# Performance work log

Hardware: AMD Instinct MI355X
Metric: run time of the kernel (lower is better)

## Reference

```python
import jax, jax.numpy as jnp
import numpy as np

B, CD, NF, V, D = 16384, 13, 26, 100000, 64
BOT = [256, 128]
TOP = [512, 256, 128]
NUM_EMB = NF + 1            # 27 (bottom output + 26 categorical)
NUM_INTER = NUM_EMB * (NUM_EMB - 1) // 2  # 351
TOP_IN = NUM_INTER + NUM_EMB * D          # 2079
BN_INV = 1.0 / np.sqrt(1.0 + 1e-5)        # eval-mode BatchNorm: running_mean=0, running_var=1


def _lin(key, fan_in, fan_out):
    kw, kb = jax.random.split(key)
    s = 1.0 / np.sqrt(fan_in)
    W = jax.random.uniform(kw, (fan_in, fan_out), minval=-s, maxval=s, dtype=jnp.float32)
    b = jax.random.uniform(kb, (fan_out,), minval=-s, maxval=s, dtype=jnp.float32)
    return W, b


def setup_inputs() -> dict:
    key = jax.random.key(0)
    ks = jax.random.split(key, 16)
    continuous = jax.random.normal(ks[0], (B, CD), dtype=jnp.float32)
    cat_idx = jax.random.randint(ks[1], (B, NF), 0, V, dtype=jnp.int32)
    emb_tables = jax.random.normal(ks[2], (NF, V, D), dtype=jnp.float32)  # nn.Embedding init ~ N(0,1)
    W1, b1 = _lin(ks[3], CD, BOT[0]);   g1 = jnp.ones((BOT[0],)); be1 = jnp.zeros((BOT[0],))
    W2, b2 = _lin(ks[4], BOT[0], BOT[1]); g2 = jnp.ones((BOT[1],)); be2 = jnp.zeros((BOT[1],))
    W3, b3 = _lin(ks[5], BOT[1], D)
    W4, b4 = _lin(ks[6], TOP_IN, TOP[0]); g4 = jnp.ones((TOP[0],)); be4 = jnp.zeros((TOP[0],))
    W5, b5 = _lin(ks[7], TOP[0], TOP[1]); g5 = jnp.ones((TOP[1],)); be5 = jnp.zeros((TOP[1],))
    W6, b6 = _lin(ks[8], TOP[1], TOP[2]); g6 = jnp.ones((TOP[2],)); be6 = jnp.zeros((TOP[2],))
    W7, b7 = _lin(ks[9], TOP[2], 1)
    return dict(continuous=continuous, cat_idx=cat_idx, emb_tables=emb_tables,
                W1=W1, b1=b1, g1=g1, be1=be1, W2=W2, b2=b2, g2=g2, be2=be2, W3=W3, b3=b3,
                W4=W4, b4=b4, g4=g4, be4=be4, W5=W5, b5=b5, g5=g5, be5=be5,
                W6=W6, b6=b6, g6=g6, be6=be6, W7=W7, b7=b7)


def _bn(x, g, b):
    # eval-mode BatchNorm1d with running_mean=0, running_var=1
    return g * (x * BN_INV) + b


def reference(continuous, cat_idx, emb_tables,
              W1, b1, g1, be1, W2, b2, g2, be2, W3, b3,
              W4, b4, g4, be4, W5, b5, g5, be5, W6, b6, g6, be6, W7, b7):
    # Bottom MLP: 13 -> 256 -> 128 -> 64
    h = jax.nn.relu(_bn(continuous @ W1 + b1, g1, be1))
    h = jax.nn.relu(_bn(h @ W2 + b2, g2, be2))
    bottom = h @ W3 + b3                         # [B, D]

    # Embedding gather: one table per categorical feature
    emb = emb_tables[jnp.arange(NF), cat_idx]    # [B, NF, D]
    all_emb = jnp.concatenate([bottom[:, None, :], emb], axis=1)  # [B, 27, D]

    # Pairwise dot-product interactions via one bmm + triu gather
    Z = jnp.einsum('bnd,bmd->bnm', all_emb, all_emb)              # [B, 27, 27]
    iu, ju = np.triu_indices(NUM_EMB, k=1)                        # row-major i<j (matches torch loop order)
    inter = Z[:, iu, ju]                                          # [B, 351]

    top_in = jnp.concatenate([inter, all_emb.reshape(all_emb.shape[0], -1)], axis=1)  # [B, 2079]

    # Top MLP: 2079 -> 512 -> 256 -> 128 -> 1
    t = jax.nn.relu(_bn(top_in @ W4 + b4, g4, be4))
    t = jax.nn.relu(_bn(t @ W5 + b5, g5, be5))
    t = jax.nn.relu(_bn(t @ W6 + b6, g6, be6))
    scores = t @ W7 + b7                                          # [B, 1]
    return scores
```

## Files before the change

kernel.cpp:

```cpp
#include <hip/hip_runtime.h>
#include <stdint.h>
#include <stddef.h>

#define BATCH   16384
#define CDIM    13
#define NFEAT   26
#define VROWS   100000
#define EDIM    64
#define NEMB    27
#define NINTER  351
#define TOPIN   2079
#define KP4     2112
#define BN_INVF 0.9999950000374997f

typedef __attribute__((ext_vector_type(8)))  __bf16 bf16x8;
typedef __attribute__((ext_vector_type(4)))  float  f32x4;
typedef __attribute__((ext_vector_type(16))) float  f32x16;
typedef __attribute__((ext_vector_type(4)))  uint32_t uint4v;

__device__ __forceinline__ uint32_t f2bf(float f){
  uint32_t u = __float_as_uint(f);
  return (u + 0x7fffu + ((u >> 16) & 1u)) >> 16;
}
__device__ __forceinline__ float bf2f(uint32_t h){ return __uint_as_float(h << 16); }
__device__ __forceinline__ uint32_t pack2(float a, float b){
  return f2bf(a) | (f2bf(b) << 16);
}
__device__ __forceinline__ void async_load16(const void* g, void* l){
  __builtin_amdgcn_global_load_lds(
      (const __attribute__((address_space(1))) uint32_t*)g,
      (__attribute__((address_space(3))) uint32_t*)l, 16, 0, 0);
}
__device__ __forceinline__ int rswz(int row){ return ((row ^ (row >> 3)) & 7) << 3; }

__device__ __forceinline__ void transpose_tile(
    float (*tile)[65], const float* __restrict__ src, unsigned short* __restrict__ dst,
    int K, int N, int Kpad, int remap, int kb, int nb){
  int k0 = kb*64, n0 = nb*64, t = threadIdx.x;
  int srcBase = remap ? ((k0 < 1728) ? (k0 + 351) : (k0 - 1728)) : k0;
  #pragma unroll 4
  for(int p = 0; p < 16; p++){
    int kr = p*4 + (t >> 6), nc = t & 63;
    float v = 0.f;
    if(k0 + kr < K && (n0 + nc) < N) v = src[(size_t)(srcBase + kr) * N + n0 + nc];
    tile[kr][nc] = v;
  }
  __syncthreads();
  #pragma unroll 4
  for(int p = 0; p < 16; p++){
    int nr = p*4 + (t >> 6), kc = t & 63;
    if(k0 + kc < Kpad && (n0 + nr) < N)
      dst[(size_t)(n0 + nr) * Kpad + k0 + kc] = (unsigned short)f2bf(tile[kc][nr]);
  }
}

__global__ __launch_bounds__(256) void prep(
    const float* __restrict__ W1, const float* __restrict__ W2, const float* __restrict__ W3,
    const float* __restrict__ W4, const float* __restrict__ W5, const float* __restrict__ W6,
    unsigned short* __restrict__ W1t, unsigned short* __restrict__ W2t,
    unsigned short* __restrict__ W3t, unsigned short* __restrict__ W4t,
    unsigned short* __restrict__ W5t, unsigned short* __restrict__ W6t){
  __shared__ float tile[64][65];
  int bid = blockIdx.x;
  if(bid < 264){ transpose_tile(tile, W4, W4t, TOPIN, 512, KP4, 1, bid % 33, bid / 33); }
  else if(bid < 296){ int r = bid-264; transpose_tile(tile, W5, W5t, 512, 256, 512, 0, r % 8, r / 8); }
  else if(bid < 304){ int r = bid-296; transpose_tile(tile, W6, W6t, 256, 128, 256, 0, r % 4, r / 4); }
  else if(bid < 312){ int r = bid-304; transpose_tile(tile, W2, W2t, 256, 128, 256, 0, r % 4, r / 4); }
  else if(bid < 314){ int r = bid-312; transpose_tile(tile, W3, W3t, 128, 64, 128, 0, r, 0); }
  else               { int r = bid-314; transpose_tile(tile, W1, W1t, CDIM, 256, 32, 0, 0, r); }
}

__global__ __launch_bounds__(256) void bottom_interact(
    const float* __restrict__ cont, const int* __restrict__ cat_idx,
    const float* __restrict__ emb,
    const unsigned short* __restrict__ W1t, const unsigned short* __restrict__ W2t,
    const unsigned short* __restrict__ W3t,
    const float* __restrict__ b1, const float* __restrict__ g1, const float* __restrict__ be1,
    const float* __restrict__ b2, const float* __restrict__ g2, const float* __restrict__ be2,
    const float* __restrict__ b3,
    unsigned short* __restrict__ top_in){
  __shared__ unsigned short h1hi[16*256];
  __shared__ unsigned short h1lo[16*256];
  __shared__ unsigned short h2hi[16*128];
  __shared__ unsigned short h2lo[16*128];
  __shared__ unsigned short bot_s[16*64];
  __shared__ unsigned short inter_s[16][352];
  int t = threadIdx.x, w = t >> 6, l = t & 63;
  int m0 = blockIdx.x * 16;
  int lr = l & 15, lg = l >> 4, lk = lg * 8;
  int r = l & 31, h = l >> 5;
  bool activeB = (r >= 1 && r < NEMB);

  int idx4[4];
  #pragma unroll
  for(int s = 0; s < 4; s++){
    int b = m0 + w*4 + s;
    idx4[s] = activeB ? cat_idx[b*NFEAT + (r-1)] : 0;
  }

  bf16x8 axh, axl;
  {
    uint32_t uh[4], ul[4];
    #pragma unroll
    for(int p = 0; p < 4; p++){
      float x0 = 0.f, x1 = 0.f;
      int k0 = lk + 2*p;
      if(k0 < CDIM)     x0 = cont[(size_t)(m0 + lr)*CDIM + k0];
      if(k0 + 1 < CDIM) x1 = cont[(size_t)(m0 + lr)*CDIM + k0 + 1];
      uint32_t h0 = f2bf(x0), h1b = f2bf(x1);
      uh[p] = h0 | (h1b << 16);
      ul[p] = f2bf(x0 - bf2f(h0)) | (f2bf(x1 - bf2f(h1b)) << 16);
    }
    uint4v vh, vl;
    #pragma unroll
    for(int e = 0; e < 4; e++){ vh[e] = uh[e]; vl[e] = ul[e]; }
    axh = __builtin_bit_cast(bf16x8, vh);
    axl = __builtin_bit_cast(bf16x8, vl);
  }

  {
    #pragma unroll
    for(int nt = 0; nt < 4; nt++){
      int n = w*64 + nt*16 + lr;
      bf16x8 bw = *(const bf16x8*)(W1t + (size_t)n*32 + lk);
      f32x4 acc;
      #pragma unroll
      for(int e = 0; e < 4; e++) acc[e] = 0.f;
      acc = __builtin_amdgcn_mfma_f32_16x16x32_bf16(axh, bw, acc, 0, 0, 0);
      acc = __builtin_amdgcn_mfma_f32_16x16x32_bf16(axl, bw, acc, 0, 0, 0);
      float sc = g1[n]*BN_INVF, bo = be1[n], bi = b1[n];
      #pragma unroll
      for(int q = 0; q < 4; q++){
        int ro = lg*4 + q;
        float y = fmaxf(sc*(acc[q] + bi) + bo, 0.f);
        uint32_t hb = f2bf(y);
        int idx = ro*256 + (n ^ rswz(ro));
        h1hi[idx] = (unsigned short)hb;
        h1lo[idx] = (unsigned short)f2bf(y - bf2f(hb));
      }
    }
  }
  __syncthreads();

  {
    f32x4 acc[2];
    #pragma unroll
    for(int nt = 0; nt < 2; nt++)
      #pragma unroll
      for(int e = 0; e < 4; e++) acc[nt][e] = 0.f;
    for(int ks = 0; ks < 8; ks++){
      bf16x8 bw[2];
      #pragma unroll
      for(int nt = 0; nt < 2; nt++){
        int n = w*32 + nt*16 + lr;
        bw[nt] = *(const bf16x8*)(W2t + (size_t)n*256 + ks*32 + lk);
      }
      int ai = lr*256 + ((ks*32 + lk) ^ rswz(lr));
      bf16x8 ah = *(const bf16x8*)(h1hi + ai);
      bf16x8 al = *(const bf16x8*)(h1lo + ai);
      #pragma unroll
      for(int nt = 0; nt < 2; nt++){
        acc[nt] = __builtin_amdgcn_mfma_f32_16x16x32_bf16(ah, bw[nt], acc[nt], 0, 0, 0);
        acc[nt] = __builtin_amdgcn_mfma_f32_16x16x32_bf16(al, bw[nt], acc[nt], 0, 0, 0);
      }
    }
    #pragma unroll
    for(int nt = 0; nt < 2; nt++){
      int n = w*32 + nt*16 + lr;
      float sc = g2[n]*BN_INVF, bo = be2[n], bi = b2[n];
      #pragma unroll
      for(int q = 0; q < 4; q++){
        int ro = lg*4 + q;
        float y = fmaxf(sc*(acc[nt][q] + bi) + bo, 0.f);
        uint32_t hb = f2bf(y);
        int idx = ro*128 + (n ^ rswz(ro));
        h2hi[idx] = (unsigned short)hb;
        h2lo[idx] = (unsigned short)f2bf(y - bf2f(hb));
      }
    }
  }
  __syncthreads();

  {
    f32x4 acc;
    #pragma unroll
    for(int e = 0; e < 4; e++) acc[e] = 0.f;
    int n = w*16 + lr;
    for(int ks = 0; ks < 4; ks++){
      bf16x8 bw = *(const bf16x8*)(W3t + (size_t)n*128 + ks*32 + lk);
      int ai = lr*128 + ((ks*32 + lk) ^ rswz(lr));
      bf16x8 ah = *(const bf16x8*)(h2hi + ai);
      bf16x8 al = *(const bf16x8*)(h2lo + ai);
      acc = __builtin_amdgcn_mfma_f32_16x16x32_bf16(ah, bw, acc, 0, 0, 0);
      acc = __builtin_amdgcn_mfma_f32_16x16x32_bf16(al, bw, acc, 0, 0, 0);
    }
    float bi = b3[n];
    #pragma unroll
    for(int q = 0; q < 4; q++){
      int ro = lg*4 + q;
      bot_s[ro*64 + n] = (unsigned short)f2bf(acc[q] + bi);
    }
  }
  __syncthreads();

  for(int s = 0; s < 4; s++){
    int sb = w*4 + s;
    int b = m0 + sb;
    uint4v q[4];
    if(r == 0){
      #pragma unroll
      for(int p = 0; p < 4; p++)
        q[p] = *(const uint4v*)(bot_s + sb*64 + h*8 + p*16);
    } else if(activeB){
      const float* src = emb + ((size_t)(r-1)*VROWS + (size_t)idx4[s])*64;
      #pragma unroll
      for(int p = 0; p < 4; p++){
        int k0 = h*8 + p*16;
        float4 v0 = *(const float4*)(src + k0);
        float4 v1 = *(const float4*)(src + k0 + 4);
        q[p][0] = pack2(v0.x, v0.y); q[p][1] = pack2(v0.z, v0.w);
        q[p][2] = pack2(v1.x, v1.y); q[p][3] = pack2(v1.z, v1.w);
      }
    } else {
      #pragma unroll
      for(int p = 0; p < 4; p++){ q[p][0]=0; q[p][1]=0; q[p][2]=0; q[p][3]=0; }
    }
    if(r < NEMB){
      #pragma unroll
      for(int p = 0; p < 4; p++)
        *(uint4v*)(top_in + (size_t)b*KP4 + r*64 + h*8 + p*16) = q[p];
    }
    f32x16 acc;
    #pragma unroll
    for(int i = 0; i < 16; i++) acc[i] = 0.f;
    #pragma unroll
    for(int p = 0; p < 4; p++){
      bf16x8 a = __builtin_bit_cast(bf16x8, q[p]);
      acc = __builtin_amdgcn_mfma_f32_32x32x16_bf16(a, a, acc, 0, 0, 0);
    }
    if(r < NEMB){
      #pragma unroll
      for(int qq = 0; qq < 16; qq++){
        int i = (qq & 3) + 8*(qq >> 2) + 4*h;
        if(i < r){
          int p = i*(53 - i)/2 + (r - i - 1);
          inter_s[sb][p] = (unsigned short)f2bf(acc[qq]);
        }
      }
    }
    asm volatile("s_waitcnt lgkmcnt(0)" ::: "memory");
    size_t basei = (size_t)b*KP4 + 1728;
    for(int t0 = l; t0 < 176; t0 += 64){
      uint32_t lo = inter_s[sb][2*t0];
      uint32_t hi = (2*t0 + 1 < NINTER) ? (uint32_t)inter_s[sb][2*t0 + 1] : 0u;
      *(uint32_t*)(top_in + basei + 2*t0) = lo | (hi << 16);
    }
    if(l < 16) *(uint32_t*)(top_in + (size_t)b*KP4 + 2080 + 2*l) = 0;
  }
}

template<int KSTEPS, int NB>
__global__ __launch_bounds__(512, 2) void gemm_deep(
    const unsigned short* __restrict__ A, int sA,
    const unsigned short* __restrict__ Bw, int sB,
    const float* __restrict__ bias, const float* __restrict__ gg,
    const float* __restrict__ be,
    unsigned short* __restrict__ out, int sOut){
  __shared__ char smem[3*49152];
  int nwg = gridDim.x;
  int bid = blockIdx.x;
  int lin = (bid & 7) * (nwg >> 3) + (bid >> 3);
  int m0 = (lin / NB) * 256, n0 = (lin % NB) * 128;
  int t = threadIdx.x, w = t >> 6, l = t & 63;
  int wr = (w >> 1) * 64, wc = (w & 1) * 64;
  int l31 = l & 31, l5 = l >> 5;
  f32x16 acc[2][2];
  #pragma unroll
  for(int i = 0; i < 2; i++)
    #pragma unroll
    for(int j = 0; j < 2; j++)
      #pragma unroll
      for(int e = 0; e < 16; e++) acc[i][j][e] = 0.f;

  const unsigned short* g[6];
  int ldsOff[6];
  #pragma unroll
  for(int i = 0; i < 6; i++){
    if(i < 4){
      int o = i*8192 + t*16;
      int row = o >> 7;
      int cb  = (o & 127) ^ ((row & 7) << 4);
      g[i] = A + (size_t)(m0 + row)*sA + (cb >> 1);
      ldsOff[i] = o;
    } else {
      int o = (i-4)*8192 + t*16;
      int row = o >> 7;
      int cb  = (o & 127) ^ ((row & 7) << 4);
      g[i] = Bw + (size_t)(n0 + row)*sB + (cb >> 1);
      ldsOff[i] = 32768 + o;
    }
  }
  int swz = (l31 & 7) << 4;

  #pragma unroll
  for(int i = 0; i < 6; i++) async_load16(g[i], smem + ldsOff[i]);
  #pragma unroll
  for(int i = 0; i < 6; i++) async_load16(g[i] + 64, smem + 49152 + ldsOff[i]);
  asm volatile("s_waitcnt vmcnt(6)" ::: "memory");
  __builtin_amdgcn_s_barrier();

  for(int kt = 0; kt < KSTEPS; kt++){
    int cur = kt % 3;
    int nxt2 = (kt + 2) % 3;
    int ksrc = (kt + 2 < KSTEPS) ? (kt + 2) : (KSTEPS - 1);
    const char* bA = smem + cur*49152;
    const char* bB = bA + 32768;
    #pragma unroll
    for(int ph = 0; ph < 2; ph++){
      if(ph == 0){
        #pragma unroll
        for(int i = 0; i < 3; i++)
          async_load16(g[i] + ksrc*64, smem + nxt2*49152 + ldsOff[i]);
      } else {
        #pragma unroll
        for(int i = 3; i < 6; i++)
          async_load16(g[i] + ksrc*64, smem + nxt2*49152 + ldsOff[i]);
      }
      bf16x8 af[2][2], bfr[2][2];
      #pragma unroll
      for(int ks = 0; ks < 2; ks++){
        int ko = ((ph*2 + ks)*32 + l5*16) ^ swz;
        #pragma unroll
        for(int mt = 0; mt < 2; mt++)
          af[ks][mt]  = *(const bf16x8*)(bA + (wr + mt*32 + l31)*128 + ko);
        #pragma unroll
        for(int nt = 0; nt < 2; nt++)
          bfr[ks][nt] = *(const bf16x8*)(bB + (wc + nt*32 + l31)*128 + ko);
      }
      if(ph == 1) asm volatile("s_waitcnt vmcnt(6)" ::: "memory");
      __builtin_amdgcn_s_barrier();
      __builtin_amdgcn_s_setprio(1);
      #pragma unroll
      for(int ks = 0; ks < 2; ks++)
        #pragma unroll
        for(int mt = 0; mt < 2; mt++)
          #pragma unroll
          for(int nt = 0; nt < 2; nt++)
            acc[mt][nt] = __builtin_amdgcn_mfma_f32_32x32x16_bf16(af[ks][mt], bfr[ks][nt], acc[mt][nt], 0, 0, 0);
      __builtin_amdgcn_s_setprio(0);
      __builtin_amdgcn_s_barrier();
    }
  }

  #pragma unroll
  for(int mt = 0; mt < 2; mt++){
    #pragma unroll
    for(int nt = 0; nt < 2; nt++){
      int col = n0 + wc + nt*32 + l31;
      float sc = gg[col]*BN_INVF, bo = be[col], bi = bias[col];
      #pragma unroll
      for(int reg = 0; reg < 16; reg++){
        int rowf = (reg & 3) + 8*(reg >> 2) + 4*l5;
        int row = m0 + wr + mt*32 + rowf;
        float y = fmaxf(sc*(acc[mt][nt][reg] + bi) + bo, 0.f);
        out[(size_t)row*sOut + col] = (unsigned short)f2bf(y);
      }
    }
  }
}

__global__ __launch_bounds__(256) void gemm_tail(
    const unsigned short* __restrict__ h4,
    const unsigned short* __restrict__ W5t,
    const float* __restrict__ b5, const float* __restrict__ g5, const float* __restrict__ be5,
    const unsigned short* __restrict__ W6t,
    const float* __restrict__ b6, const float* __restrict__ g6, const float* __restrict__ be6,
    const float* __restrict__ W7, const float* __restrict__ b7,
    float* __restrict__ scores){
  __shared__ char smem[74752];
  unsigned short* h5 = (unsigned short*)(smem + 40960);
  float* pscore = (float*)(smem + 73728);
  int t = threadIdx.x, w = t >> 6, l = t & 63;
  int m0 = blockIdx.x * 64;
  int lr = l & 15;
  int o1 = ((l >> 4) * 16) ^ ((l & 7) << 4);

  f32x4 acc5[4][4];
  #pragma unroll
  for(int i = 0; i < 4; i++)
    #pragma unroll
    for(int j = 0; j < 4; j++)
      #pragma unroll
      for(int e = 0; e < 4; e++) acc5[i][j][e] = 0.f;

  const unsigned short* gA[2]; int ldsA[2];
  #pragma unroll
  for(int i = 0; i < 2; i++){
    int o = i*4096 + t*16;
    int row = o >> 7;
    int cb = (o & 127) ^ ((row & 7) << 4);
    gA[i] = h4 + (size_t)(m0 + row)*512 + (cb >> 1);
    ldsA[i] = o;
  }
  const unsigned short* gB[8]; int ldsB[8];
  #pragma unroll
  for(int i = 0; i < 8; i++){
    int o = i*4096 + t*16;
    int row = o >> 7;
    int cb = (o & 127) ^ ((row & 7) << 4);
    gB[i] = W5t + (size_t)row*512 + (cb >> 1);
    ldsB[i] = 8192 + o;
  }

  for(int kt = 0; kt < 8; kt++){
    #pragma unroll
    for(int i = 0; i < 2; i++) async_load16(gA[i] + kt*64, smem + ldsA[i]);
    #pragma unroll
    for(int i = 0; i < 8; i++) async_load16(gB[i] + kt*64, smem + ldsB[i]);
    __syncthreads();
    #pragma unroll
    for(int ks = 0; ks < 2; ks++){
      int ko = o1 ^ (ks << 6);
      bf16x8 af[4], bfr[4];
      #pragma unroll
      for(int x = 0; x < 4; x++){
        af[x]  = *(const bf16x8*)(smem + (x*16 + lr)*128 + ko);
        bfr[x] = *(const bf16x8*)(smem + 8192 + (w*64 + x*16 + lr)*128 + ko);
      }
      #pragma unroll
      for(int tr = 0; tr < 4; tr++)
        #pragma unroll
        for(int tc = 0; tc < 4; tc++)
          acc5[tr][tc] = __builtin_amdgcn_mfma_f32_16x16x32_bf16(af[tr], bfr[tc], acc5[tr][tc], 0, 0, 0);
    }
    __syncthreads();
  }

  #pragma unroll
  for(int i = 0; i < 8; i++){
    int o = i*4096 + t*16;
    int row = o >> 8;
    int cb = (o & 255) ^ ((row & 15) << 4);
    async_load16(W6t + (size_t)row*256 + (cb >> 1), smem + o);
  }
  #pragma unroll
  for(int tc = 0; tc < 4; tc++){
    int c = w*64 + tc*16 + lr;
    float sc = g5[c]*BN_INVF, bo = be5[c], bi = b5[c];
    #pragma unroll
    for(int tr = 0; tr < 4; tr++){
      #pragma unroll
      for(int qq = 0; qq < 4; qq++){
        int row = tr*16 + (l >> 4)*4 + qq;
        float y = fmaxf(sc*(acc5[tr][tc][qq] + bi) + bo, 0.f);
        h5[row*256 + (c ^ rswz(row))] = (unsigned short)f2bf(y);
      }
    }
  }
  __syncthreads();

  f32x4 acc6[4][2];
  #pragma unroll
  for(int i = 0; i < 4; i++)
    #pragma unroll
    for(int j = 0; j < 2; j++)
      #pragma unroll
      for(int e = 0; e < 4; e++) acc6[i][j][e] = 0.f;
  int lk = (l >> 4) * 8;
  int lk2 = (l >> 4) * 16;
  #pragma unroll
  for(int half = 0; half < 2; half++){
    if(half == 1){
      __syncthreads();
      #pragma unroll
      for(int i = 0; i < 8; i++){
        int o = i*4096 + t*16;
        int row = o >> 8;
        int cb = (o & 255) ^ ((row & 15) << 4);
        async_load16(W6t + (size_t)row*256 + 128 + (cb >> 1), smem + o);
      }
      __syncthreads();
    }
    #pragma unroll
    for(int ks = 0; ks < 4; ks++){
      bf16x8 af6[4], bfr6[2];
      #pragma unroll
      for(int mt = 0; mt < 4; mt++){
        int row = mt*16 + lr;
        af6[mt] = *(const bf16x8*)(h5 + row*256 + ((half*128 + ks*32 + lk) ^ rswz(row)));
      }
      #pragma unroll
      for(int nt = 0; nt < 2; nt++){
        int row = w*32 + nt*16 + lr;
        bfr6[nt] = *(const bf16x8*)(smem + row*256 + ((ks*64 + lk2) ^ (lr << 4)));
      }
      #pragma unroll
      for(int mt = 0; mt < 4; mt++)
        #pragma unroll
        for(int nt = 0; nt < 2; nt++)
          acc6[mt][nt] = __builtin_amdgcn_mfma_f32_16x16x32_bf16(af6[mt], bfr6[nt], acc6[mt][nt], 0, 0, 0);
    }
  }

  float pr[16];
  #pragma unroll
  for(int nt = 0; nt < 2; nt++){
    int c = w*32 + nt*16 + lr;
    float sc = g6[c]*BN_INVF, bo = be6[c], bi = b6[c];
    float w7c = W7[c];
    #pragma unroll
    for(int mt = 0; mt < 4; mt++){
      #pragma unroll
      for(int qq = 0; qq < 4; qq++){
        float v = fmaxf(sc*(acc6[mt][nt][qq] + bi) + bo, 0.f) * w7c;
        if(nt == 0) pr[mt*4 + qq] = v; else pr[mt*4 + qq] += v;
      }
    }
  }
  #pragma unroll
  for(int mask = 1; mask < 16; mask <<= 1){
    #pragma unroll
    for(int i = 0; i < 16; i++) pr[i] += __shfl_xor(pr[i], mask, 64);
  }
  if(lr == 0){
    #pragma unroll
    for(int mt = 0; mt < 4; mt++)
      #pragma unroll
      for(int qq = 0; qq < 4; qq++)
        pscore[w*64 + mt*16 + (l >> 4)*4 + qq] = pr[mt*4 + qq];
  }
  __syncthreads();
  if(t < 64){
    float s = b7[0] + pscore[t] + pscore[64 + t] + pscore[128 + t] + pscore[192 + t];
    scores[m0 + t] = s;
  }
}

static inline size_t alignup(size_t x){ return (x + 255) & ~(size_t)255; }

extern "C" void kernel_launch(void* const* d_in, const int* in_sizes, int n_in,
                              void* d_out, int out_size, void* d_ws, size_t ws_size,
                              hipStream_t stream){
  const float* cont = (const float*)d_in[0];
  const int*   cat  = (const int*)  d_in[1];
  const float* emb  = (const float*)d_in[2];
  const float* W1 = (const float*)d_in[3],  *b1 = (const float*)d_in[4];
  const float* g1 = (const float*)d_in[5],  *be1= (const float*)d_in[6];
  const float* W2 = (const float*)d_in[7],  *b2 = (const float*)d_in[8];
  const float* g2 = (const float*)d_in[9],  *be2= (const float*)d_in[10];
  const float* W3 = (const float*)d_in[11], *b3 = (const float*)d_in[12];
  const float* W4 = (const float*)d_in[13], *b4 = (const float*)d_in[14];
  const float* g4 = (const float*)d_in[15], *be4= (const float*)d_in[16];
  const float* W5 = (const float*)d_in[17], *b5 = (const float*)d_in[18];
  const float* g5 = (const float*)d_in[19], *be5= (const float*)d_in[20];
  const float* W6 = (const float*)d_in[21], *b6 = (const float*)d_in[22];
  const float* g6 = (const float*)d_in[23], *be6= (const float*)d_in[24];
  const float* W7 = (const float*)d_in[25], *b7 = (const float*)d_in[26];

  char* ws = (char*)d_ws;
  unsigned short* W1t  = (unsigned short*)ws; ws += alignup((size_t)256*32*2);
  unsigned short* W2t  = (unsigned short*)ws; ws += alignup((size_t)128*256*2);
  unsigned short* W3t  = (unsigned short*)ws; ws += alignup((size_t)64*128*2);
  unsigned short* topi = (unsigned short*)ws; ws += alignup((size_t)BATCH*KP4*2);
  unsigned short* W4t  = (unsigned short*)ws; ws += alignup((size_t)512*KP4*2);
  unsigned short* W5t  = (unsigned short*)ws; ws += alignup((size_t)256*512*2);
  unsigned short* W6t  = (unsigned short*)ws; ws += alignup((size_t)128*256*2);
  unsigned short* h4   = (unsigned short*)ws; ws += alignup((size_t)BATCH*512*2);
  (void)ws_size; (void)n_in; (void)in_sizes; (void)out_size;

  hipLaunchKernelGGL(prep, dim3(318), dim3(256), 0, stream,
                     W1, W2, W3, W4, W5, W6,
                     W1t, W2t, W3t, W4t, W5t, W6t);
  hipLaunchKernelGGL(bottom_interact, dim3(BATCH/16), dim3(256), 0, stream,
                     cont, cat, emb, W1t, W2t, W3t,
                     b1, g1, be1, b2, g2, be2, b3, topi);
  hipLaunchKernelGGL((gemm_deep<33, 4>), dim3(256), dim3(512), 0, stream,
                     topi, KP4, W4t, KP4, b4, g4, be4, h4, 512);
  hipLaunchKernelGGL(gemm_tail, dim3(256), dim3(256), 0, stream,
                     h4, W5t, b5, g5, be5, W6t, b6, g6, be6, W7, b7, (float*)d_out);
}
```

Measured before the change: 119.1 us.

## Switch deep GEMM to 16x16x32 MFMA tiles and prefetch embedding rows

The deep GEMM's inner loop moves from 32x32x16 MFMA fragments to 16x16x32 ones, with a 4x4 accumulator grid per wave, new LDS read offsets and a new epilogue mapping. The intent is better MFMA throughput and fewer LDS fragment reads per k-step. Separately, the embedding gather loop now software-prefetches the next sample's table row into registers so global load latency overlaps the interaction MFMA work. Both changes raise register pressure, which may hurt occupancy.

```diff
diff --git a/kernel.cpp b/kernel.cpp
--- a/kernel.cpp
+++ b/kernel.cpp
@@ -203,6 +203,16 @@
   }
   __syncthreads();
 
+  float4 raw[8];
+  if(activeB){
+    const float* src = emb + ((size_t)(r-1)*VROWS + (size_t)idx4[0])*64;
+    #pragma unroll
+    for(int p = 0; p < 4; p++){
+      raw[2*p]   = *(const float4*)(src + h*8 + p*16);
+      raw[2*p+1] = *(const float4*)(src + h*8 + p*16 + 4);
+    }
+  }
+  #pragma unroll
   for(int s = 0; s < 4; s++){
     int sb = w*4 + s;
     int b = m0 + sb;
@@ -212,18 +222,22 @@
       for(int p = 0; p < 4; p++)
         q[p] = *(const uint4v*)(bot_s + sb*64 + h*8 + p*16);
     } else if(activeB){
-      const float* src = emb + ((size_t)(r-1)*VROWS + (size_t)idx4[s])*64;
       #pragma unroll
       for(int p = 0; p < 4; p++){
-        int k0 = h*8 + p*16;
-        float4 v0 = *(const float4*)(src + k0);
-        float4 v1 = *(const float4*)(src + k0 + 4);
-        q[p][0] = pack2(v0.x, v0.y); q[p][1] = pack2(v0.z, v0.w);
-        q[p][2] = pack2(v1.x, v1.y); q[p][3] = pack2(v1.z, v1.w);
+        q[p][0] = pack2(raw[2*p].x, raw[2*p].y); q[p][1] = pack2(raw[2*p].z, raw[2*p].w);
+        q[p][2] = pack2(raw[2*p+1].x, raw[2*p+1].y); q[p][3] = pack2(raw[2*p+1].z, raw[2*p+1].w);
       }
     } else {
       #pragma unroll
       for(int p = 0; p < 4; p++){ q[p][0]=0; q[p][1]=0; q[p][2]=0; q[p][3]=0; }
+    }
+    if(s < 3 && activeB){
+      const float* src = emb + ((size_t)(r-1)*VROWS + (size_t)idx4[s+1])*64;
+      #pragma unroll
+      for(int p = 0; p < 4; p++){
+        raw[2*p]   = *(const float4*)(src + h*8 + p*16);
+        raw[2*p+1] = *(const float4*)(src + h*8 + p*16 + 4);
+      }
     }
     if(r < NEMB){
       #pragma unroll
@@ -273,14 +287,13 @@
   int m0 = (lin / NB) * 256, n0 = (lin % NB) * 128;
   int t = threadIdx.x, w = t >> 6, l = t & 63;
   int wr = (w >> 1) * 64, wc = (w & 1) * 64;
-  int l31 = l & 31, l5 = l >> 5;
-  f32x16 acc[2][2];
-  #pragma unroll
-  for(int i = 0; i < 2; i++)
-    #pragma unroll
-    for(int j = 0; j < 2; j++)
-      #pragma unroll
-      for(int e = 0; e < 16; e++) acc[i][j][e] = 0.f;
+  f32x4 acc[4][4];
+  #pragma unroll
+  for(int i = 0; i < 4; i++)
+    #pragma unroll
+    for(int j = 0; j < 4; j++)
+      #pragma unroll
+      for(int e = 0; e < 4; e++) acc[i][j][e] = 0.f;
 
   const unsigned short* g[6];
   int ldsOff[6];
@@ -300,7 +313,8 @@
       ldsOff[i] = 32768 + o;
     }
   }
-  int swz = (l31 & 7) << 4;
+  int lr = l & 15;
+  int o1 = ((l >> 4) * 16) ^ ((l & 7) << 4);
 
   #pragma unroll
   for(int i = 0; i < 6; i++) async_load16(g[i], smem + ldsOff[i]);
@@ -316,54 +330,60 @@
     const char* bA = smem + cur*49152;
     const char* bB = bA + 32768;
     #pragma unroll
-    for(int ph = 0; ph < 2; ph++){
-      if(ph == 0){
-        #pragma unroll
-        for(int i = 0; i < 3; i++)
-          async_load16(g[i] + ksrc*64, smem + nxt2*49152 + ldsOff[i]);
-      } else {
-        #pragma unroll
-        for(int i = 3; i < 6; i++)
-          async_load16(g[i] + ksrc*64, smem + nxt2*49152 + ldsOff[i]);
-      }
-      bf16x8 af[2][2], bfr[2][2];
-      #pragma unroll
-      for(int ks = 0; ks < 2; ks++){
-        int ko = ((ph*2 + ks)*32 + l5*16) ^ swz;
-        #pragma unroll
-        for(int mt = 0; mt < 2; mt++)
-          af[ks][mt]  = *(const bf16x8*)(bA + (wr + mt*32 + l31)*128 + ko);
-        #pragma unroll
-        for(int nt = 0; nt < 2; nt++)
-          bfr[ks][nt] = *(const bf16x8*)(bB + (wc + nt*32 + l31)*128 + ko);
-      }
-      if(ph == 1) asm volatile("s_waitcnt vmcnt(6)" ::: "memory");
+    for(int i = 0; i < 3; i++)
+      async_load16(g[i] + ksrc*64, smem + nxt2*49152 + ldsOff[i]);
+    {
+      bf16x8 af[4], bfr[4];
+      #pragma unroll
+      for(int x = 0; x < 4; x++){
+        af[x]  = *(const bf16x8*)(bA + (wr + x*16 + lr)*128 + o1);
+        bfr[x] = *(const bf16x8*)(bB + (wc + x*16 + lr)*128 + o1);
+      }
       __builtin_amdgcn_s_barrier();
       __builtin_amdgcn_s_setprio(1);
       #pragma unroll
-      for(int ks = 0; ks < 2; ks++)
+      for(int tr = 0; tr < 4; tr++)
         #pragma unroll
-        for(int mt = 0; mt < 2; mt++)
-          #pragma unroll
-          for(int nt = 0; nt < 2; nt++)
-            acc[mt][nt] = __builtin_amdgcn_mfma_f32_32x32x16_bf16(af[ks][mt], bfr[ks][nt], acc[mt][nt], 0, 0, 0);
+        for(int tc = 0; tc < 4; tc++)
+          acc[tr][tc] = __builtin_amdgcn_mfma_f32_16x16x32_bf16(af[tr], bfr[tc], acc[tr][tc], 0, 0, 0);
       __builtin_amdgcn_s_setprio(0);
+    }
+    __builtin_amdgcn_s_barrier();
+    #pragma unroll
+    for(int i = 3; i < 6; i++)
+      async_load16(g[i] + ksrc*64, smem + nxt2*49152 + ldsOff[i]);
+    {
+      bf16x8 af[4], bfr[4];
+      int ko = o1 ^ 64;
+      #pragma unroll
+      for(int x = 0; x < 4; x++){
+        af[x]  = *(const bf16x8*)(bA + (wr + x*16 + lr)*128 + ko);
+        bfr[x] = *(const bf16x8*)(bB + (wc + x*16 + lr)*128 + ko);
+      }
+      asm volatile("s_waitcnt vmcnt(6)" ::: "memory");
       __builtin_amdgcn_s_barrier();
-    }
-  }
-
-  #pragma unroll
-  for(int mt = 0; mt < 2; mt++){
-    #pragma unroll
-    for(int nt = 0; nt < 2; nt++){
-      int col = n0 + wc + nt*32 + l31;
-      float sc = gg[col]*BN_INVF, bo = be[col], bi = bias[col];
-      #pragma unroll
-      for(int reg = 0; reg < 16; reg++){
-        int rowf = (reg & 3) + 8*(reg >> 2) + 4*l5;
-        int row = m0 + wr + mt*32 + rowf;
-        float y = fmaxf(sc*(acc[mt][nt][reg] + bi) + bo, 0.f);
-        out[(size_t)row*sOut + col] = (unsigned short)f2bf(y);
+      __builtin_amdgcn_s_setprio(1);
+      #pragma unroll
+      for(int tr = 0; tr < 4; tr++)
+        #pragma unroll
+        for(int tc = 0; tc < 4; tc++)
+          acc[tr][tc] = __builtin_amdgcn_mfma_f32_16x16x32_bf16(af[tr], bfr[tc], acc[tr][tc], 0, 0, 0);
+      __builtin_amdgcn_s_setprio(0);
+    }
+    __builtin_amdgcn_s_barrier();
+  }
+
+  #pragma unroll
+  for(int tc = 0; tc < 4; tc++){
+    int n = n0 + wc + tc*16 + lr;
+    float sc = gg[n]*BN_INVF, bo = be[n], bi = bias[n];
+    #pragma unroll
+    for(int tr = 0; tr < 4; tr++){
+      int mb = m0 + wr + tr*16 + (l >> 4)*4;
+      #pragma unroll
+      for(int qq = 0; qq < 4; qq++){
+        float y = fmaxf(sc*(acc[tr][tc][qq] + bi) + bo, 0.f);
+        out[(size_t)(mb + qq)*sOut + n] = (unsigned short)f2bf(y);
       }
     }
   }
```

Result: faster. 116.4 us, median of 2 (-2.3%).
